# Performance work log

Measured on AMD Instinct MI355X. Metric: run time of the kernel, lower is better.

## Reference

```python
import math
import jax, jax.numpy as jnp
import numpy as np

D_MODEL = 1024
NUM_HEAD = 16
HEAD_DIM = 64
B = 4
S = 1024


def setup_inputs() -> dict:
    key = jax.random.key(0)
    ks = jax.random.split(key, 11)
    scale = 1.0 / math.sqrt(D_MODEL)
    inp = {
        "x": jax.random.normal(ks[0], (B, S, D_MODEL), dtype=jnp.float32),
        "y": jax.random.normal(ks[1], (B, S, D_MODEL), dtype=jnp.float32),
        "mask": jnp.zeros((S, S), dtype=jnp.float32),
        "Wq": jax.random.uniform(ks[2], (D_MODEL, D_MODEL), jnp.float32, -scale, scale),
        "bq": jax.random.uniform(ks[3], (D_MODEL,), jnp.float32, -scale, scale),
        "Wk": jax.random.uniform(ks[4], (D_MODEL, D_MODEL), jnp.float32, -scale, scale),
        "bk": jax.random.uniform(ks[5], (D_MODEL,), jnp.float32, -scale, scale),
        "Wv": jax.random.uniform(ks[6], (D_MODEL, D_MODEL), jnp.float32, -scale, scale),
        "bv": jax.random.uniform(ks[7], (D_MODEL,), jnp.float32, -scale, scale),
        "Wo": jax.random.uniform(ks[8], (D_MODEL, D_MODEL), jnp.float32, -scale, scale),
        "bo": jax.random.uniform(ks[9], (D_MODEL,), jnp.float32, -scale, scale),
    }
    return inp


def _split_heads(t):
    # (B, S, D) -> (B, H, S, hd)
    b, s, _ = t.shape
    return t.reshape(b, s, NUM_HEAD, HEAD_DIM).transpose(0, 2, 1, 3)


def reference(x, y, mask, Wq, bq, Wk, bk, Wv, bv, Wo, bo):
    q = _split_heads(y @ Wq.T + bq)  # (B, H, S, hd)
    k = _split_heads(x @ Wk.T + bk)
    v = _split_heads(x @ Wv.T + bv)
    scaled = jnp.einsum("bhqd,bhkd->bhqk", q, k) / math.sqrt(HEAD_DIM)
    # torch: scaled.permute(1,0,2,3) + mask  -> (H, B, S, S); second permute is a no-op
    scaled = scaled.transpose(1, 0, 2, 3) + mask
    attention = jax.nn.softmax(scaled, axis=-1)
    attention = jnp.where(jnp.isnan(attention), 0.0, attention)
    # torch sum(dim=1) on (H, B, S, S) sums over BATCH -> (H, S, S)
    attention = jnp.sum(attention, axis=1)
    # broadcast matmul: (H, S, S) @ (B, H, S, hd) -> (B, H, S, hd)
    V = jnp.einsum("hqk,bhkd->bhqd", attention, v)
    V = V.transpose(0, 2, 1, 3).reshape(B, S, NUM_HEAD * HEAD_DIM)
    return V @ Wo.T + bo
```

## Files before the change

kernel.cpp:

```cpp
#include <hip/hip_runtime.h>

typedef unsigned short u16;
typedef unsigned int   u32;
typedef __attribute__((ext_vector_type(8))) short short8;
typedef __attribute__((ext_vector_type(4))) float floatx4;

#define DEV static __device__ __forceinline__

constexpr int S_  = 1024;
constexpr int Dm  = 1024;
constexpr int HD  = 64;


DEV u16 f2b(float f) {
  u32 u = __builtin_bit_cast(u32, f);
  u = u + 0x7fffu + ((u >> 16) & 1u);
  return (u16)(u >> 16);
}
DEV float b2f(u16 h) { u32 u = ((u32)h) << 16; return __builtin_bit_cast(float, u); }

DEV void gld16(const u16* g, u16* l) {
  __builtin_amdgcn_global_load_lds(
      (const __attribute__((address_space(1))) u32*)g,
      (__attribute__((address_space(3))) u32*)l, 16, 0, 0);
}

template<int ROWS, int NT>
DEV void stage_tile(const u16* src, long stride, long kOff, u16* lds, int tid) {
  constexpr int NBLK = ROWS * 8;
  constexpr int NISS = NBLK / NT;
  static_assert(NBLK % NT == 0, "");
  int w = tid >> 6;
  #pragma unroll
  for (int i = 0; i < NISS; ++i) {
    int bi = i * NT + tid;
    int m  = bi >> 3;
    int kb = (bi & 7) ^ (m & 7);
    const u16* g = src + (long)m * stride + kOff + (kb << 3);
    u16* l = lds + ((long)(i * NT + (w << 6)) << 3);
    gld16(g, l);
  }
}

DEV short8 read_frag(const u16* lds, int m, int kb) {
  int off = (m << 6) + ((kb ^ (m & 7)) << 3);
  return *(const short8*)(lds + off);
}

DEV floatx4 mfma16(short8 a, short8 b, floatx4 c) {
  return __builtin_amdgcn_mfma_f32_16x16x32_bf16(a, b, c, 0, 0, 0);
}


struct CvtArgs { const float* s[6]; u16* d[6]; };

__global__ __launch_bounds__(256)
void cvt_all(CvtArgs a) {
  int b = blockIdx.x;
  int t, lb;
  if (b < 4096)      { t = 0; lb = b; }
  else if (b < 8192) { t = 1; lb = b - 4096; }
  else               { t = 2 + ((b - 8192) >> 10); lb = (b - 8192) & 1023; }
  int i = (lb * 256 + (int)threadIdx.x) * 4;
  float4 v = *(const float4*)(a.s[t] + i);
  u32 lo = (u32)f2b(v.x) | ((u32)f2b(v.y) << 16);
  u32 hi = (u32)f2b(v.z) | ((u32)f2b(v.w) << 16);
  uint2 o; o.x = lo; o.y = hi;
  *(uint2*)(a.d[t] + i) = o;
}


__global__ __launch_bounds__(256)
void emask_prep(const float* __restrict__ mask, u16* __restrict__ em,
                u16* __restrict__ emr) {
  __shared__ u16 lp[8 * 1024];
  int tid = threadIdx.x;
  long q0 = (long)blockIdx.x * 8;
  #pragma unroll
  for (int rr = 0; rr < 8; ++rr) {
    long q = q0 + rr;
    float4 v = *(const float4*)(mask + q * 1024 + tid * 4);
    u16 e0 = f2b(__expf(v.x)), e1 = f2b(__expf(v.y));
    u16 e2 = f2b(__expf(v.z)), e3 = f2b(__expf(v.w));
    u32 lo = (u32)e0 | ((u32)e1 << 16);
    u32 hi = (u32)e2 | ((u32)e3 << 16);
    uint2 o; o.x = lo; o.y = hi;
    *(uint2*)(em + q * 1024 + tid * 4) = o;
    int k = tid * 4;
    u16 es[4] = {e0, e1, e2, e3};
    #pragma unroll
    for (int j = 0; j < 4; ++j) {
      int kk = k + j;
      lp[rr * 1024 + ((kk & 15) << 6) + (kk >> 4)] = es[j];
    }
  }
  __syncthreads();
  #pragma unroll
  for (int jj = 0; jj < 4; ++jj) {
    int o = jj * 2048 + tid * 8;
    uint4 v = *(const uint4*)(lp + o);
    *(uint4*)(emr + q0 * 1024 + o) = v;
  }
}


struct QkvArgs { const u16* A[3]; const u16* W[3]; const float* bias[3]; u16* C[3]; };

__global__ __launch_bounds__(256, 2)
void gemm_qkv(QkvArgs args) {
  constexpr int CPAD = 136;
  __shared__ u16 smem[128 * CPAD];
  u16* lA = smem;
  u16* lB = smem + 8192;
  int tid = threadIdx.x, lane = tid & 63, w = tid >> 6;
  int wm = w & 1, wn = w >> 1;
  int sel = blockIdx.z;
  bool vt = (sel == 2);
  float scl = (sel == 0) ? 0.125f : 1.0f;
  long mBase = (long)blockIdx.y * 128;
  long nBase = (long)blockIdx.x * 128;
  const u16* Ab = args.A[sel] + mBase * (long)Dm;
  const u16* Bb = args.W[sel] + nBase * (long)Dm;
  const float* bias = args.bias[sel];
  u16* C = args.C[sel];

  floatx4 acc[4][4];
  #pragma unroll
  for (int i = 0; i < 4; ++i)
    #pragma unroll
    for (int j = 0; j < 4; ++j) acc[i][j] = floatx4{0.f, 0.f, 0.f, 0.f};

  for (int kt = 0; kt < Dm; kt += 64) {
    __syncthreads();
    stage_tile<128, 256>(Ab, Dm, kt, lA, tid);
    stage_tile<128, 256>(Bb, Dm, kt, lB, tid);
    __syncthreads();
    #pragma unroll
    for (int ks = 0; ks < 2; ++ks) {
      short8 af[4], bf[4];
      #pragma unroll
      for (int mi = 0; mi < 4; ++mi)
        af[mi] = read_frag(lA, wm*64 + mi*16 + (lane & 15), ks*4 + (lane >> 4));
      #pragma unroll
      for (int ni = 0; ni < 4; ++ni)
        bf[ni] = read_frag(lB, wn*64 + ni*16 + (lane & 15), ks*4 + (lane >> 4));
      #pragma unroll
      for (int mi = 0; mi < 4; ++mi)
        #pragma unroll
        for (int ni = 0; ni < 4; ++ni)
          acc[mi][ni] = mfma16(af[mi], bf[ni], acc[mi][ni]);
    }
  }

  __syncthreads();
  #pragma unroll
  for (int mi = 0; mi < 4; ++mi) {
    int rowb = wm*64 + mi*16 + ((lane >> 4) << 2);
    #pragma unroll
    for (int ni = 0; ni < 4; ++ni) {
      int col = wn*64 + ni*16 + (lane & 15);
      float bv = bias[nBase + col];
      #pragma unroll
      for (int r = 0; r < 4; ++r) {
        float v = (acc[mi][ni][r] + bv) * scl;
        if (!vt) smem[(rowb + r) * CPAD + col] = f2b(v);
        else     smem[col * CPAD + (rowb + r)] = f2b(v);
      }
    }
  }
  __syncthreads();
  #pragma unroll
  for (int i = 0; i < 8; ++i) {
    int idx = (i * 256 + tid) * 8;
    int r0 = idx >> 7, c0 = idx & 127;
    uint4 v = *(const uint4*)(smem + r0 * CPAD + c0);
    if (!vt) {
      *(uint4*)(C + (mBase + r0) * (long)Dm + nBase + c0) = v;
    } else {
      long m = mBase + c0;
      long ad = ((m >> 10) << 20) + ((nBase + r0) << 10) + (m & 1023);
      *(uint4*)(C + ad) = v;
    }
  }
}


constexpr int MO_BF16 = 0, MO_F32 = 1;

template<int BM, int BN, int WM, int WN, int MODE, bool BIAS, bool ZBH>
__global__ __launch_bounds__(WM*WN*64, 2)
void gemm_bt(const u16* __restrict__ A, const u16* __restrict__ Bmat,
             const float* __restrict__ bias, void* __restrict__ C,
             int K, int ldc) {
  constexpr int NT   = WM * WN * 64;
  constexpr int MI   = BM / WM / 16;
  constexpr int NI   = BN / WN / 16;
  constexpr int WROW = BM / WM;
  constexpr int WCOL = BN / WN;
  constexpr int STG  = (BM + BN) * 64;
  constexpr int CPAD = BN + 8;
  constexpr int CSZ  = BM * CPAD;
  constexpr int SM   = (MODE == MO_F32) ? STG : (STG > CSZ ? STG : CSZ);
  __shared__ u16 smem[SM];
  u16* lA = smem;
  u16* lB = smem + BM * 64;

  int tid = threadIdx.x, lane = tid & 63, w = tid >> 6;
  int wm = w % WM, wn = w / WM;
  long mBase = (long)blockIdx.y * BM;
  long nBase = (long)blockIdx.x * BN;
  long aOff = 0, bOff = 0, cOff = 0;
  if (ZBH) {
    int z = blockIdx.z, bz = z >> 4, h = z & 15;
    aOff = (long)h << 20;
    bOff = (long)z << 16;
    cOff = ((long)bz << 20) + h * HD;
  }
  const u16* Ab = A + aOff + mBase * (long)K;
  const u16* Bb = Bmat + bOff + nBase * (long)K;

  floatx4 acc[MI][NI];
  #pragma unroll
  for (int i = 0; i < MI; ++i)
    #pragma unroll
    for (int j = 0; j < NI; ++j) acc[i][j] = floatx4{0.f, 0.f, 0.f, 0.f};

  for (int kt = 0; kt < K; kt += 64) {
    __syncthreads();
    stage_tile<BM, NT>(Ab, K, kt, lA, tid);
    stage_tile<BN, NT>(Bb, K, kt, lB, tid);
    __syncthreads();
    #pragma unroll
    for (int ks = 0; ks < 2; ++ks) {
      short8 af[MI], bf[NI];
      #pragma unroll
      for (int mi = 0; mi < MI; ++mi)
        af[mi] = read_frag(lA, wm*WROW + mi*16 + (lane & 15), ks*4 + (lane >> 4));
      #pragma unroll
      for (int ni = 0; ni < NI; ++ni)
        bf[ni] = read_frag(lB, wn*WCOL + ni*16 + (lane & 15), ks*4 + (lane >> 4));
      #pragma unroll
      for (int mi = 0; mi < MI; ++mi)
        #pragma unroll
        for (int ni = 0; ni < NI; ++ni)
          acc[mi][ni] = mfma16(af[mi], bf[ni], acc[mi][ni]);
    }
  }

  if (MODE == MO_F32) {
    #pragma unroll
    for (int mi = 0; mi < MI; ++mi) {
      int rowb = wm*WROW + mi*16 + ((lane >> 4) << 2);
      #pragma unroll
      for (int ni = 0; ni < NI; ++ni) {
        int col = wn*WCOL + ni*16 + (lane & 15);
        long n = nBase + col;
        float bv = BIAS ? bias[n] : 0.f;
        #pragma unroll
        for (int r = 0; r < 4; ++r)
          ((float*)C)[cOff + (mBase + rowb + r) * (long)ldc + n] = acc[mi][ni][r] + bv;
      }
    }
  } else {
    __syncthreads();
    #pragma unroll
    for (int mi = 0; mi < MI; ++mi) {
      int rowb = wm*WROW + mi*16 + ((lane >> 4) << 2);
      #pragma unroll
      for (int ni = 0; ni < NI; ++ni) {
        int col = wn*WCOL + ni*16 + (lane & 15);
        float bv = BIAS ? bias[nBase + col] : 0.f;
        #pragma unroll
        for (int r = 0; r < 4; ++r)
          smem[(rowb + r) * CPAD + col] = f2b(acc[mi][ni][r] + bv);
      }
    }
    __syncthreads();
    constexpr int TOT = BM * BN;
    #pragma unroll
    for (int i = 0; i < TOT / (NT * 8); ++i) {
      int idx = (i * NT + tid) * 8;
      int r0 = idx / BN, c0 = idx % BN;
      uint4 v = *(const uint4*)(smem + r0 * CPAD + c0);
      *(uint4*)((u16*)C + cOff + (mBase + r0) * (long)ldc + nBase + c0) = v;
    }
  }
}


__global__ __launch_bounds__(256, 2)
void attn_stats(const u16* __restrict__ Q, const u16* __restrict__ Kw,
                const u16* __restrict__ emr, float* __restrict__ lPart) {
  __shared__ u16 lQ[128 * 64];
  __shared__ u16 lK[128 * 64];
  int tid = threadIdx.x, lane = tid & 63, w = tid >> 6;
  int qT = blockIdx.x, h = blockIdx.y, z = blockIdx.z;
  int b = z >> 2, c = z & 3;
  const u16* Qb = Q + ((long)b << 20) + h * HD + (long)qT * 128 * Dm;
  const u16* Kb = Kw + ((long)b << 20) + h * HD + (long)c * 256 * Dm;

  stage_tile<128, 256>(Qb, Dm, 0, lQ, tid);
  __syncthreads();
  short8 af[2][2];
  #pragma unroll
  for (int mi = 0; mi < 2; ++mi)
    #pragma unroll
    for (int ks = 0; ks < 2; ++ks)
      af[mi][ks] = read_frag(lQ, w*32 + mi*16 + (lane & 15), ks*4 + (lane >> 4));

  float lsum[2][4];
  #pragma unroll
  for (int mi = 0; mi < 2; ++mi)
    #pragma unroll
    for (int r = 0; r < 4; ++r) lsum[mi][r] = 0.f;

  for (int kt = 0; kt < 2; ++kt) {
    __syncthreads();
    stage_tile<128, 256>(Kb + (long)kt * 128 * Dm, Dm, 0, lK, tid);
    __syncthreads();
    floatx4 sc[2][8];
    #pragma unroll
    for (int mi = 0; mi < 2; ++mi)
      #pragma unroll
      for (int ni = 0; ni < 8; ++ni) sc[mi][ni] = floatx4{0.f, 0.f, 0.f, 0.f};
    #pragma unroll
    for (int ks = 0; ks < 2; ++ks) {
      short8 bf[8];
      #pragma unroll
      for (int ni = 0; ni < 8; ++ni)
        bf[ni] = read_frag(lK, ni*16 + (lane & 15), ks*4 + (lane >> 4));
      #pragma unroll
      for (int mi = 0; mi < 2; ++mi)
        #pragma unroll
        for (int ni = 0; ni < 8; ++ni)
          sc[mi][ni] = mfma16(af[mi][ks], bf[ni], sc[mi][ni]);
    }
    int q0w = qT*128 + w*32;
    int iBase = (c*256 + kt*128) >> 4;
    #pragma unroll
    for (int mi = 0; mi < 2; ++mi)
      #pragma unroll
      for (int r = 0; r < 4; ++r) {
        int q = q0w + mi*16 + ((lane >> 4) << 2) + r;
        uint4 ev = *(const uint4*)(emr + ((long)q << 10) + ((lane & 15) << 6) + iBase);
        const u16* e8 = (const u16*)&ev;
        float a = 0.f;
        #pragma unroll
        for (int ni = 0; ni < 8; ++ni)
          a += __expf(sc[mi][ni][r]) * b2f(e8[ni]);
        lsum[mi][r] += a;
      }
  }
  #pragma unroll
  for (int mi = 0; mi < 2; ++mi)
    #pragma unroll
    for (int r = 0; r < 4; ++r) {
      float l = lsum[mi][r];
      #pragma unroll
      for (int off = 1; off < 16; off <<= 1) l += __shfl_xor(l, off);
      if ((lane & 15) == 0) {
        int q = qT*128 + w*32 + mi*16 + ((lane >> 4) << 2) + r;
        lPart[(long)c * 65536 + ((long)(b * 16 + h) << 10) + q] = l;
      }
    }
}


__global__ __launch_bounds__(256, 2)
void attn_probs(const u16* __restrict__ Q, const u16* __restrict__ Kw,
                const u16* __restrict__ em, const float* __restrict__ lPart,
                u16* __restrict__ att) {
  constexpr int CPAD = 136;
  __shared__ u16 smem[128 * CPAD];
  __shared__ float lL[128];
  u16* lQ = smem;
  u16* lK = smem + 8192;
  int tid = threadIdx.x, lane = tid & 63, w = tid >> 6;
  int wm = w & 1, wn = w >> 1;
  int kT = blockIdx.x, qT = blockIdx.y, h = blockIdx.z;
  long q0 = (long)qT * 128, k0 = (long)kT * 128;

  floatx4 pa[4][4];
  #pragma unroll
  for (int i = 0; i < 4; ++i)
    #pragma unroll
    for (int j = 0; j < 4; ++j) pa[i][j] = floatx4{0.f, 0.f, 0.f, 0.f};

  for (int b = 0; b < 4; ++b) {
    __syncthreads();
    stage_tile<128, 256>(Q + ((long)b << 20) + h * HD + q0 * Dm, Dm, 0, lQ, tid);
    stage_tile<128, 256>(Kw + ((long)b << 20) + h * HD + k0 * Dm, Dm, 0, lK, tid);
    if (tid < 128) {
      long base = ((long)(b * 16 + h) << 10) + q0 + tid;
      float l = 0.f;
      #pragma unroll
      for (int cch = 0; cch < 4; ++cch) l += lPart[(long)cch * 65536 + base];
      lL[tid] = (l > 0.f) ? 1.f / l : 0.f;
    }
    __syncthreads();
    floatx4 sc[4][4];
    #pragma unroll
    for (int i = 0; i < 4; ++i)
      #pragma unroll
      for (int j = 0; j < 4; ++j) sc[i][j] = floatx4{0.f, 0.f, 0.f, 0.f};
    #pragma unroll
    for (int ks = 0; ks < 2; ++ks) {
      short8 af[4], bf[4];
      #pragma unroll
      for (int mi = 0; mi < 4; ++mi)
        af[mi] = read_frag(lQ, wm*64 + mi*16 + (lane & 15), ks*4 + (lane >> 4));
      #pragma unroll
      for (int ni = 0; ni < 4; ++ni)
        bf[ni] = read_frag(lK, wn*64 + ni*16 + (lane & 15), ks*4 + (lane >> 4));
      #pragma unroll
      for (int mi = 0; mi < 4; ++mi)
        #pragma unroll
        for (int ni = 0; ni < 4; ++ni)
          sc[mi][ni] = mfma16(af[mi], bf[ni], sc[mi][ni]);
    }
    #pragma unroll
    for (int mi = 0; mi < 4; ++mi)
      #pragma unroll
      for (int r = 0; r < 4; ++r) {
        int qq = wm*64 + mi*16 + ((lane >> 4) << 2) + r;
        float li = lL[qq];
        #pragma unroll
        for (int ni = 0; ni < 4; ++ni)
          pa[mi][ni][r] += __expf(sc[mi][ni][r]) * li;
      }
  }

  __syncthreads();
  #pragma unroll
  for (int mi = 0; mi < 4; ++mi)
    #pragma unroll
    for (int ni = 0; ni < 4; ++ni) {
      int kc = wn*64 + ni*16 + (lane & 15);
      #pragma unroll
      for (int r = 0; r < 4; ++r) {
        int qq = wm*64 + mi*16 + ((lane >> 4) << 2) + r;
        smem[qq * CPAD + kc] = f2b(pa[mi][ni][r]);
      }
    }
  __syncthreads();
  #pragma unroll
  for (int i = 0; i < 8; ++i) {
    int idx = (i * 256 + tid) * 8;
    int r0 = idx >> 7, c0 = idx & 127;
    uint4 v  = *(const uint4*)(smem + r0 * CPAD + c0);
    uint4 ev = *(const uint4*)(em + (q0 + r0) * S_ + k0 + c0);
    const u16* pv = (const u16*)&v;
    const u16* ee = (const u16*)&ev;
    u16 ov[8];
    #pragma unroll
    for (int j = 0; j < 8; ++j) ov[j] = f2b(b2f(pv[j]) * b2f(ee[j]));
    *(uint4*)(att + ((long)h << 20) + (q0 + r0) * S_ + k0 + c0) = *(uint4*)ov;
  }
}


extern "C" void kernel_launch(void* const* d_in, const int* in_sizes, int n_in,
                              void* d_out, int out_size, void* d_ws, size_t ws_size,
                              hipStream_t stream) {
  const float* x    = (const float*)d_in[0];
  const float* y    = (const float*)d_in[1];
  const float* mask = (const float*)d_in[2];
  const float* Wq   = (const float*)d_in[3];
  const float* bq   = (const float*)d_in[4];
  const float* Wk   = (const float*)d_in[5];
  const float* bk   = (const float*)d_in[6];
  const float* Wv   = (const float*)d_in[7];
  const float* bv   = (const float*)d_in[8];
  const float* Wo   = (const float*)d_in[9];
  const float* bo   = (const float*)d_in[10];

  char* ws = (char*)d_ws;
  const long MB = 1024 * 1024;
  u16*  Qw   = (u16*)(ws + 0);
  u16*  Kw   = (u16*)(ws + 8 * MB);
  u16*  Vt   = (u16*)(ws + 16 * MB);
  u16*  attv = (u16*)(ws + 24 * MB);
  float* lPart = (float*)(ws + 24 * MB);
  u16*  em   = (u16*)(ws + 25 * MB);
  u16*  emr  = (u16*)(ws + 27 * MB);
  u16*  Wob  = (u16*)(ws + 33 * MB);
  u16*  att  = (u16*)(ws + 35 * MB);
  u16*  yb   = (u16*)(ws + 35 * MB);
  u16*  xb   = (u16*)(ws + 43 * MB);
  u16*  Wqb  = (u16*)(ws + 51 * MB);
  u16*  Wkb  = (u16*)(ws + 53 * MB);
  u16*  Wvb  = (u16*)(ws + 55 * MB);

  dim3 blk(256);
  CvtArgs ca;
  ca.s[0] = y;  ca.s[1] = x;  ca.s[2] = Wq;  ca.s[3] = Wk;  ca.s[4] = Wv;  ca.s[5] = Wo;
  ca.d[0] = yb; ca.d[1] = xb; ca.d[2] = Wqb; ca.d[3] = Wkb; ca.d[4] = Wvb; ca.d[5] = Wob;
  cvt_all<<<dim3(12288), blk, 0, stream>>>(ca);
  emask_prep<<<dim3(128), blk, 0, stream>>>(mask, em, emr);

  QkvArgs qa;
  qa.A[0] = yb;  qa.A[1] = xb;  qa.A[2] = xb;
  qa.W[0] = Wqb; qa.W[1] = Wkb; qa.W[2] = Wvb;
  qa.bias[0] = bq; qa.bias[1] = bk; qa.bias[2] = bv;
  qa.C[0] = Qw;  qa.C[1] = Kw;  qa.C[2] = Vt;
  gemm_qkv<<<dim3(8, 32, 3), blk, 0, stream>>>(qa);

  attn_stats<<<dim3(8, 16, 16), blk, 0, stream>>>(Qw, Kw, emr, lPart);
  attn_probs<<<dim3(8, 8, 16), blk, 0, stream>>>(Qw, Kw, em, lPart, att);

  gemm_bt<128,64,2,2,MO_BF16,false,true><<<dim3(1, 8, 64), blk, 0, stream>>>(att, Vt, nullptr, attv, 1024, 1024);
  gemm_bt<64,128,2,2,MO_F32,true,false><<<dim3(8, 64), blk, 0, stream>>>(attv, Wob, bo, d_out, 1024, 1024);
}
```

Measured before the change: 250.8 us.

## Double-buffer K/Q tiles in attention stats and probs kernels, halve key chunks

Both attention kernels now stage the next tile into a second LDS buffer while the current one is computed, with one barrier per iteration in place of two. attn_stats splits keys into 2 chunks of 512 rather than 4 of 256, halving its grid and the partial sums attn_probs must add. attn_probs loads all four batches' inverse row sums once up front. The changes aim to hide global-load latency and cut synchronisation, at the cost of more LDS per block, a dropped min-blocks occupancy hint, and fewer blocks in attn_stats.

```diff
diff --git a/kernel.cpp b/kernel.cpp
--- a/kernel.cpp
+++ b/kernel.cpp
@@ -288,19 +288,21 @@
 }
 
 
-__global__ __launch_bounds__(256, 2)
+__global__ __launch_bounds__(256)
 void attn_stats(const u16* __restrict__ Q, const u16* __restrict__ Kw,
                 const u16* __restrict__ emr, float* __restrict__ lPart) {
   __shared__ u16 lQ[128 * 64];
-  __shared__ u16 lK[128 * 64];
+  __shared__ u16 lK[2][128 * 64];
   int tid = threadIdx.x, lane = tid & 63, w = tid >> 6;
   int qT = blockIdx.x, h = blockIdx.y, z = blockIdx.z;
-  int b = z >> 2, c = z & 3;
+  int b = z >> 1, c = z & 1;
   const u16* Qb = Q + ((long)b << 20) + h * HD + (long)qT * 128 * Dm;
-  const u16* Kb = Kw + ((long)b << 20) + h * HD + (long)c * 256 * Dm;
+  const u16* Kb = Kw + ((long)b << 20) + h * HD + (long)c * 512 * Dm;
 
   stage_tile<128, 256>(Qb, Dm, 0, lQ, tid);
-  __syncthreads();
+  stage_tile<128, 256>(Kb, Dm, 0, lK[0], tid);
+  __syncthreads();
+
   short8 af[2][2];
   #pragma unroll
   for (int mi = 0; mi < 2; ++mi)
@@ -314,10 +316,10 @@
     #pragma unroll
     for (int r = 0; r < 4; ++r) lsum[mi][r] = 0.f;
 
-  for (int kt = 0; kt < 2; ++kt) {
-    __syncthreads();
-    stage_tile<128, 256>(Kb + (long)kt * 128 * Dm, Dm, 0, lK, tid);
-    __syncthreads();
+  for (int kt = 0; kt < 4; ++kt) {
+    if (kt < 3)
+      stage_tile<128, 256>(Kb + (long)(kt + 1) * 128 * Dm, Dm, 0, lK[(kt + 1) & 1], tid);
+    const u16* lKc = lK[kt & 1];
     floatx4 sc[2][8];
     #pragma unroll
     for (int mi = 0; mi < 2; ++mi)
@@ -328,7 +330,7 @@
       short8 bf[8];
       #pragma unroll
       for (int ni = 0; ni < 8; ++ni)
-        bf[ni] = read_frag(lK, ni*16 + (lane & 15), ks*4 + (lane >> 4));
+        bf[ni] = read_frag(lKc, ni*16 + (lane & 15), ks*4 + (lane >> 4));
       #pragma unroll
       for (int mi = 0; mi < 2; ++mi)
         #pragma unroll
@@ -336,7 +338,7 @@
           sc[mi][ni] = mfma16(af[mi][ks], bf[ni], sc[mi][ni]);
     }
     int q0w = qT*128 + w*32;
-    int iBase = (c*256 + kt*128) >> 4;
+    int iBase = (c*512 + kt*128) >> 4;
     #pragma unroll
     for (int mi = 0; mi < 2; ++mi)
       #pragma unroll
@@ -350,6 +352,7 @@
           a += __expf(sc[mi][ni][r]) * b2f(e8[ni]);
         lsum[mi][r] += a;
       }
+    if (kt < 3) __syncthreads();
   }
   #pragma unroll
   for (int mi = 0; mi < 2; ++mi)
@@ -366,20 +369,30 @@
 }
 
 
-__global__ __launch_bounds__(256, 2)
+__global__ __launch_bounds__(256)
 void attn_probs(const u16* __restrict__ Q, const u16* __restrict__ Kw,
                 const u16* __restrict__ em, const float* __restrict__ lPart,
                 u16* __restrict__ att) {
   constexpr int CPAD = 136;
-  __shared__ u16 smem[128 * CPAD];
-  __shared__ float lL[128];
-  u16* lQ = smem;
-  u16* lK = smem + 8192;
+  __shared__ u16 smem[4 * 8192];
+  __shared__ float lL[512];
   int tid = threadIdx.x, lane = tid & 63, w = tid >> 6;
   int wm = w & 1, wn = w >> 1;
   int kT = blockIdx.x, qT = blockIdx.y, h = blockIdx.z;
   long q0 = (long)qT * 128, k0 = (long)kT * 128;
 
+  stage_tile<128, 256>(Q + h * HD + q0 * Dm, Dm, 0, smem, tid);
+  stage_tile<128, 256>(Kw + h * HD + k0 * Dm, Dm, 0, smem + 8192, tid);
+  #pragma unroll
+  for (int j = 0; j < 2; ++j) {
+    int t = tid + j * 256;
+    int bb = t >> 7, qq = t & 127;
+    long base = ((long)(bb * 16 + h) << 10) + q0 + qq;
+    float l = lPart[base] + lPart[65536 + base];
+    lL[t] = (l > 0.f) ? 1.f / l : 0.f;
+  }
+  __syncthreads();
+
   floatx4 pa[4][4];
   #pragma unroll
   for (int i = 0; i < 4; ++i)
@@ -387,17 +400,12 @@
     for (int j = 0; j < 4; ++j) pa[i][j] = floatx4{0.f, 0.f, 0.f, 0.f};
 
   for (int b = 0; b < 4; ++b) {
-    __syncthreads();
-    stage_tile<128, 256>(Q + ((long)b << 20) + h * HD + q0 * Dm, Dm, 0, lQ, tid);
-    stage_tile<128, 256>(Kw + ((long)b << 20) + h * HD + k0 * Dm, Dm, 0, lK, tid);
-    if (tid < 128) {
-      long base = ((long)(b * 16 + h) << 10) + q0 + tid;
-      float l = 0.f;
-      #pragma unroll
-      for (int cch = 0; cch < 4; ++cch) l += lPart[(long)cch * 65536 + base];
-      lL[tid] = (l > 0.f) ? 1.f / l : 0.f;
-    }
-    __syncthreads();
+    u16* buf = smem + (b & 1) * 16384;
+    if (b < 3) {
+      u16* nb = smem + ((b + 1) & 1) * 16384;
+      stage_tile<128, 256>(Q + ((long)(b+1) << 20) + h * HD + q0 * Dm, Dm, 0, nb, tid);
+      stage_tile<128, 256>(Kw + ((long)(b+1) << 20) + h * HD + k0 * Dm, Dm, 0, nb + 8192, tid);
+    }
     floatx4 sc[4][4];
     #pragma unroll
     for (int i = 0; i < 4; ++i)
@@ -408,10 +416,10 @@
       short8 af[4], bf[4];
       #pragma unroll
       for (int mi = 0; mi < 4; ++mi)
-        af[mi] = read_frag(lQ, wm*64 + mi*16 + (lane & 15), ks*4 + (lane >> 4));
+        af[mi] = read_frag(buf, wm*64 + mi*16 + (lane & 15), ks*4 + (lane >> 4));
       #pragma unroll
       for (int ni = 0; ni < 4; ++ni)
-        bf[ni] = read_frag(lK, wn*64 + ni*16 + (lane & 15), ks*4 + (lane >> 4));
+        bf[ni] = read_frag(buf + 8192, wn*64 + ni*16 + (lane & 15), ks*4 + (lane >> 4));
       #pragma unroll
       for (int mi = 0; mi < 4; ++mi)
         #pragma unroll
@@ -423,11 +431,12 @@
       #pragma unroll
       for (int r = 0; r < 4; ++r) {
         int qq = wm*64 + mi*16 + ((lane >> 4) << 2) + r;
-        float li = lL[qq];
+        float li = lL[(b << 7) + qq];
         #pragma unroll
         for (int ni = 0; ni < 4; ++ni)
           pa[mi][ni][r] += __expf(sc[mi][ni][r]) * li;
       }
+    if (b < 3) __syncthreads();
   }
 
   __syncthreads();
@@ -505,7 +514,7 @@
   qa.C[0] = Qw;  qa.C[1] = Kw;  qa.C[2] = Vt;
   gemm_qkv<<<dim3(8, 32, 3), blk, 0, stream>>>(qa);
 
-  attn_stats<<<dim3(8, 16, 16), blk, 0, stream>>>(Qw, Kw, emr, lPart);
+  attn_stats<<<dim3(8, 16, 8), blk, 0, stream>>>(Qw, Kw, emr, lPart);
   attn_probs<<<dim3(8, 8, 16), blk, 0, stream>>>(Qw, Kw, em, lPart, att);
 
   gemm_bt<128,64,2,2,MO_BF16,false,true><<<dim3(1, 8, 64), blk, 0, stream>>>(att, Vt, nullptr, attv, 1024, 1024);
```

Measured after the change: 252.3 us. Within noise of the previous version (+0.6%).
